# Kernel tuning notes

Measured on AMD Instinct MI355X. Metric: run time of the kernel, lower is better.

Reference implementation:

```python
import jax, jax.numpy as jnp
import numpy as np
import math

B, Q, CQ = 2, 2048, 512
H, D = 8, 64  # no_heads, c_hidden

def setup_inputs() -> dict:
    key = jax.random.key(0)
    ks = jax.random.split(key, 8)
    s = 0.02
    return {
        "q_x": jax.random.normal(ks[0], (B, Q, CQ), jnp.float32),
        "kv_x": jax.random.normal(ks[1], (B, Q, CQ), jnp.float32),
        "bias": jax.random.normal(ks[2], (B, 1, Q, Q), jnp.float32),
        "w_qkv": jax.random.normal(ks[3], (3 * H * D, CQ), jnp.float32) * s,
        "w_o": jax.random.normal(ks[4], (CQ, H * D), jnp.float32) * s,
        "b_o": jnp.zeros((CQ,), jnp.float32),
        "w_g": jax.random.normal(ks[5], (H * D, CQ), jnp.float32) * s,
        "b_g": jnp.zeros((H * D,), jnp.float32),
    }

def reference(q_x, kv_x, bias, w_qkv, w_o, b_o, w_g, b_g):
    # Fused QKV projection from q_x (kv_x is unused by the original module's _prep_qkv)
    qkv = jnp.einsum('bqc,ec->bqe', q_x, w_qkv)  # [B,Q,3*H*D]
    q, k, v = jnp.split(qkv, 3, axis=-1)
    q = q.reshape(B, Q, H, D) / math.sqrt(D)
    k = k.reshape(B, Q, H, D)
    v = v.reshape(B, Q, H, D)
    # scores + additive pairwise bias, softmax over keys
    scores = jnp.einsum('bqhd,bkhd->bhqk', q, k) + bias  # [B,H,Q,K]
    attn = jax.nn.softmax(scores, axis=-1)
    o = jnp.einsum('bhqk,bkhd->bqhd', attn, v)  # [B,Q,H,D]
    # sigmoid gating
    g = jax.nn.sigmoid(jnp.einsum('bqc,ec->bqe', q_x, w_g) + b_g).reshape(B, Q, H, D)
    o = o * g
    # output projection
    o = o.reshape(B, Q, H * D)
    return jnp.einsum('bqe,ce->bqc', o, w_o) + b_o
```

## Files before the change

### kernel.cpp

```cpp
#include <hip/hip_runtime.h>
#include <math.h>

#define B_  2
#define Q_  2048
#define CQ_ 512
#define H_  8
#define D_  64
#define M_  (B_*Q_)
#define L2E 1.44269504088896f

typedef __bf16 bf16;
typedef __bf16 bf16x4 __attribute__((ext_vector_type(4)));
typedef __bf16 bf16x8 __attribute__((ext_vector_type(8)));
typedef float  f32x4  __attribute__((ext_vector_type(4)));
typedef float  f32x16 __attribute__((ext_vector_type(16)));
typedef unsigned int u32x2 __attribute__((ext_vector_type(2)));

__device__ __forceinline__ void gl_lds16(const bf16* g, bf16* l) {
    __builtin_amdgcn_global_load_lds(
        (const __attribute__((address_space(1))) unsigned int*)g,
        (__attribute__((address_space(3))) unsigned int*)l, 16, 0, 0);
}

__device__ __forceinline__ unsigned int cvtpk_bf16(float lo, float hi) {
    unsigned int r;
    asm("v_cvt_pk_bf16_f32 %0, %1, %2" : "=v"(r) : "v"(lo), "v"(hi));
    return r;
}

#define S0 (4096*512)
#define S1 (1536*512)
#define S2 (512*512)
#define S3 (512*512)
__global__ __launch_bounds__(256)
void convert_kernel(const float* __restrict__ qx, const float* __restrict__ wqkv,
                    const float* __restrict__ wg, const float* __restrict__ wo,
                    bf16* __restrict__ qxb, bf16* __restrict__ wcat, bf16* __restrict__ wob)
{
    const long long t = (long long)blockIdx.x * 256 + threadIdx.x;
    const long long e = t * 8;
    const float* src; bf16* dst;
    if (e < S0)                { src = qx + e;                  dst = qxb + e; }
    else if (e < S0 + S1)      { src = wqkv + (e - S0);         dst = wcat + (e - S0); }
    else if (e < S0 + S1 + S2) { src = wg + (e - S0 - S1);      dst = wcat + S1 + (e - S0 - S1); }
    else                       { src = wo + (e - S0 - S1 - S2); dst = wob + (e - S0 - S1 - S2); }
    const float4 a = *(const float4*)(src);
    const float4 b = *(const float4*)(src + 4);
    bf16x8 v;
    v[0] = (bf16)a.x; v[1] = (bf16)a.y; v[2] = (bf16)a.z; v[3] = (bf16)a.w;
    v[4] = (bf16)b.x; v[5] = (bf16)b.y; v[6] = (bf16)b.z; v[7] = (bf16)b.w;
    *(bf16x8*)dst = v;
}

template<int BM, int BN, int EPI>
__global__ __launch_bounds__(256)
void gemm_bf16(const bf16* __restrict__ A, const bf16* __restrict__ W,
               const float* __restrict__ bvec, float* __restrict__ fout,
               bf16* __restrict__ qb, bf16* __restrict__ kb, bf16* __restrict__ vb,
               bf16* __restrict__ gb)
{
    constexpr int MI = BM / 32, NJ = BN / 32;
    __shared__ __align__(16) bf16 As[BM * 32];
    __shared__ __align__(16) bf16 Bs[BN * 32];

    const int t = threadIdx.x;
    const int w = t >> 6, lane = t & 63;
    const int l15 = lane & 15, quad = lane >> 4;
    const int wm = w & 1, wn = w >> 1;
    const int bm = blockIdx.x * BM;
    const int bn = blockIdx.y * BN;
    const bool swapped = (EPI == 1) || ((bn >> 9) != 2);

    f32x4 acc[MI][NJ] = {};

    const int rr = t >> 2;
    const int cc = (t & 3) * 8;

    for (int k0 = 0; k0 < 512; k0 += 32) {
        #pragma unroll
        for (int i = 0; i < BM / 64; ++i)
            gl_lds16(A + (size_t)(bm + i * 64 + rr) * 512 + k0 + cc,
                     As + (i * 64 + w * 16) * 32);
        #pragma unroll
        for (int i = 0; i < BN / 64; ++i)
            gl_lds16(W + (size_t)(bn + i * 64 + rr) * 512 + k0 + cc,
                     Bs + (i * 64 + w * 16) * 32);
        __asm__ volatile("s_waitcnt vmcnt(0)" ::: "memory");
        __syncthreads();

        bf16x8 af[MI], bfr[NJ];
        #pragma unroll
        for (int i = 0; i < MI; ++i)
            af[i] = *(const bf16x8*)(As + (wm * (BM / 2) + i * 16 + l15) * 32 + quad * 8);
        #pragma unroll
        for (int j = 0; j < NJ; ++j)
            bfr[j] = *(const bf16x8*)(Bs + (wn * (BN / 2) + j * 16 + l15) * 32 + quad * 8);
        if (swapped) {
            #pragma unroll
            for (int i = 0; i < MI; ++i)
                #pragma unroll
                for (int j = 0; j < NJ; ++j)
                    acc[i][j] = __builtin_amdgcn_mfma_f32_16x16x32_bf16(bfr[j], af[i], acc[i][j], 0, 0, 0);
        } else {
            #pragma unroll
            for (int i = 0; i < MI; ++i)
                #pragma unroll
                for (int j = 0; j < NJ; ++j)
                    acc[i][j] = __builtin_amdgcn_mfma_f32_16x16x32_bf16(af[i], bfr[j], acc[i][j], 0, 0, 0);
        }
        __syncthreads();
    }

    if (swapped) {
        #pragma unroll
        for (int i = 0; i < MI; ++i) {
            const int m = bm + wm * (BM / 2) + i * 16 + l15;
            const int b = m >> 11, qq = m & 2047;
            #pragma unroll
            for (int j = 0; j < NJ; ++j) {
                const int n0 = bn + wn * (BN / 2) + j * 16 + quad * 4;
                const f32x4 cv = acc[i][j];
                if constexpr (EPI == 1) {
                    float4 st;
                    st.x = cv[0] + bvec[n0 + 0];
                    st.y = cv[1] + bvec[n0 + 1];
                    st.z = cv[2] + bvec[n0 + 2];
                    st.w = cv[3] + bvec[n0 + 3];
                    *(float4*)(fout + (size_t)m * 512 + n0) = st;
                } else {
                    const int part = n0 >> 9;
                    if (part == 0) {
                        const int h = (n0 >> 6) & 7, d0 = n0 & 63;
                        bf16x4 q4;
                        #pragma unroll
                        for (int r = 0; r < 4; ++r) q4[r] = (bf16)(cv[r] * (0.125f * L2E));
                        *(bf16x4*)(qb + (size_t)(b * H_ + h) * (Q_ * D_) + (size_t)qq * 64 + d0) = q4;
                    } else if (part == 1) {
                        const int h = (n0 >> 6) & 7, d0 = n0 & 63;
                        const size_t off = (size_t)(b * H_ + h) * (Q_ * D_)
                            + (qq >> 6) * 4096 + ((qq >> 5) & 1) * 2048
                            + (d0 >> 4) * 512 + ((d0 >> 3) & 1) * 256
                            + (qq & 31) * 8 + (d0 & 7);
                        bf16x4 k4;
                        #pragma unroll
                        for (int r = 0; r < 4; ++r) k4[r] = (bf16)cv[r];
                        *(bf16x4*)(kb + off) = k4;
                    } else {
                        const int gcol = n0 & 511;
                        const float4 bv4 = *(const float4*)(bvec + gcol);
                        bf16x4 g4;
                        g4[0] = (bf16)(1.f / (1.f + __expf(-(cv[0] + bv4.x))));
                        g4[1] = (bf16)(1.f / (1.f + __expf(-(cv[1] + bv4.y))));
                        g4[2] = (bf16)(1.f / (1.f + __expf(-(cv[2] + bv4.z))));
                        g4[3] = (bf16)(1.f / (1.f + __expf(-(cv[3] + bv4.w))));
                        *(bf16x4*)(gb + (size_t)m * 512 + gcol) = g4;
                    }
                }
            }
        }
    } else {
        #pragma unroll
        for (int i = 0; i < MI; ++i) {
            const int m0 = bm + wm * (BM / 2) + i * 16 + quad * 4;
            const int b = m0 >> 11, qq0 = m0 & 2047;
            #pragma unroll
            for (int j = 0; j < NJ; ++j) {
                const int n = bn + wn * (BN / 2) + j * 16 + l15;
                const int h = (n >> 6) & 7, d = n & 63;
                const size_t off = (size_t)(b * H_ + h) * (Q_ * D_)
                    + (qq0 >> 6) * 4096 + (d >> 5) * 2048
                    + ((qq0 & 63) >> 4) * 512 + ((qq0 >> 3) & 1) * 256
                    + (d & 31) * 8 + (qq0 & 7);
                bf16x4 v4;
                #pragma unroll
                for (int r = 0; r < 4; ++r) v4[r] = (bf16)acc[i][j][r];
                *(bf16x4*)(vb + off) = v4;
            }
        }
    }
}

__global__ __launch_bounds__(256, 3)
void attn_part(const bf16* __restrict__ qb, const bf16* __restrict__ kf,
               const bf16* __restrict__ vf, const float* __restrict__ bias,
               bf16* __restrict__ po, float2* __restrict__ ml)
{
    __shared__ __align__(16) bf16 Ks[2][4096];
    __shared__ __align__(16) bf16 Vs[2][4096];

    const int tid  = threadIdx.x;
    const int wv   = tid >> 6, lane = tid & 63;
    const int l31  = lane & 31, b5 = lane >> 5;
    const int x    = blockIdx.x;
    const int bh   = ((x & 7) << 1) | (x >> 3);
    const int b    = bh >> 3;
    const int qg   = blockIdx.y * 128 + wv * 32 + l31;
    const int ks   = blockIdx.z;
    const int t0   = ks * 11;
    const int nt   = (ks < 2) ? 11 : 10;

    const bf16* qp = qb + ((size_t)bh * Q_ + qg) * D_;
    bf16x8 bq[4];
    #pragma unroll
    for (int c = 0; c < 4; ++c)
        bq[c] = *(const bf16x8*)(qp + c * 16 + b5 * 8);

    f32x16 acc[2] = {};
    float m_run = -INFINITY, l_run = 0.f;

    const bf16*  kfb  = kf + (size_t)bh * (Q_ * D_) + (size_t)t0 * 4096;
    const bf16*  vfb  = vf + (size_t)bh * (Q_ * D_) + (size_t)t0 * 4096;
    const float* brow = bias + ((size_t)b * Q_ + qg) * Q_ + t0 * 64;

    f32x4 nb[8];

    #pragma unroll
    for (int p = 0; p < 2; ++p) {
        gl_lds16(kfb + (wv * 2 + p) * 512 + lane * 8, Ks[0] + (wv * 2 + p) * 512);
        gl_lds16(vfb + (wv * 2 + p) * 512 + lane * 8, Vs[0] + (wv * 2 + p) * 512);
    }
    #pragma unroll
    for (int i = 0; i < 8; ++i)
        nb[i] = *(const f32x4*)(brow + (i >> 2) * 32 + (i & 3) * 8 + b5 * 4);
    __asm__ volatile("s_waitcnt vmcnt(0)" ::: "memory");
    __syncthreads();

    int cur = 0;
    #pragma unroll 1
    for (int t = 0; t < nt; ++t) {
        if (t < nt - 1) {
            const size_t off = (size_t)(t + 1) * 4096;
            #pragma unroll
            for (int p = 0; p < 2; ++p) {
                gl_lds16(kfb + off + (wv * 2 + p) * 512 + lane * 8,
                         Ks[cur ^ 1] + (wv * 2 + p) * 512);
                gl_lds16(vfb + off + (wv * 2 + p) * 512 + lane * 8,
                         Vs[cur ^ 1] + (wv * 2 + p) * 512);
            }
        }
        __asm__ volatile("" ::: "memory");

        f32x16 sv[2];
        #pragma unroll
        for (int kg = 0; kg < 2; ++kg)
            #pragma unroll
            for (int r = 0; r < 16; ++r)
                sv[kg][r] = nb[kg * 4 + (r >> 2)][r & 3] * L2E;

        if (t < nt - 1) {
            const int k0n = (t + 1) * 64;
            #pragma unroll
            for (int i = 0; i < 8; ++i)
                nb[i] = *(const f32x4*)(brow + k0n + (i >> 2) * 32 + (i & 3) * 8 + b5 * 4);
        }
        __asm__ volatile("" ::: "memory");

        const bf16* Kc = Ks[cur];
        __builtin_amdgcn_s_setprio(1);
        #pragma unroll
        for (int kg = 0; kg < 2; ++kg)
            #pragma unroll
            for (int c = 0; c < 4; ++c) {
                const bf16x8 ak = *(const bf16x8*)(Kc + kg * 2048 + c * 512 + lane * 8);
                sv[kg] = __builtin_amdgcn_mfma_f32_32x32x16_bf16(ak, bq[c], sv[kg], 0, 0, 0);
            }
        __builtin_amdgcn_s_setprio(0);

        float mx[16];
        #pragma unroll
        for (int r = 0; r < 16; ++r) mx[r] = fmaxf(sv[0][r], sv[1][r]);
        #pragma unroll
        for (int r = 0; r < 8; ++r) mx[r] = fmaxf(mx[r], mx[r + 8]);
        #pragma unroll
        for (int r = 0; r < 4; ++r) mx[r] = fmaxf(mx[r], mx[r + 4]);
        float tmax = fmaxf(fmaxf(mx[0], mx[1]), fmaxf(mx[2], mx[3]));
        tmax = fmaxf(tmax, __shfl_xor(tmax, 32, 64));

        const float mn = fmaxf(m_run, tmax);
        const float alpha = __builtin_amdgcn_exp2f(m_run - mn);
        m_run = mn;

        #pragma unroll
        for (int kg = 0; kg < 2; ++kg)
            #pragma unroll
            for (int r = 0; r < 16; ++r)
                sv[kg][r] = __builtin_amdgcn_exp2f(sv[kg][r] - mn);

        float sm[16];
        #pragma unroll
        for (int r = 0; r < 16; ++r) sm[r] = sv[0][r] + sv[1][r];
        #pragma unroll
        for (int r = 0; r < 8; ++r) sm[r] += sm[r + 8];
        #pragma unroll
        for (int r = 0; r < 4; ++r) sm[r] += sm[r + 4];
        float rsum = (sm[0] + sm[1]) + (sm[2] + sm[3]);
        rsum += __shfl_xor(rsum, 32, 64);
        l_run = l_run * alpha + rsum;
        acc[0] *= alpha;
        acc[1] *= alpha;

        bf16x8 bp[4];
        #pragma unroll
        for (int kg = 0; kg < 2; ++kg)
            #pragma unroll
            for (int h = 0; h < 2; ++h) {
                const unsigned int u  = cvtpk_bf16(sv[kg][8 * h + 0], sv[kg][8 * h + 1]);
                const unsigned int u2 = cvtpk_bf16(sv[kg][8 * h + 2], sv[kg][8 * h + 3]);
                const unsigned int vv = cvtpk_bf16(sv[kg][8 * h + 4], sv[kg][8 * h + 5]);
                const unsigned int v2 = cvtpk_bf16(sv[kg][8 * h + 6], sv[kg][8 * h + 7]);
                const u32x2 s1 = __builtin_amdgcn_permlane32_swap(u,  vv, false, false);
                const u32x2 s2 = __builtin_amdgcn_permlane32_swap(u2, v2, false, false);
                union { unsigned int w[4]; bf16x8 v8; } pkw;
                pkw.w[0] = s1[0]; pkw.w[1] = s2[0]; pkw.w[2] = s1[1]; pkw.w[3] = s2[1];
                bp[kg * 2 + h] = pkw.v8;
            }

        const bf16* Vc = Vs[cur];
        __builtin_amdgcn_s_setprio(1);
        #pragma unroll
        for (int c4 = 0; c4 < 4; ++c4) {
            #pragma unroll
            for (int dg = 0; dg < 2; ++dg) {
                const bf16x8 av = *(const bf16x8*)(Vc + dg * 2048 + c4 * 512 + lane * 8);
                acc[dg] = __builtin_amdgcn_mfma_f32_32x32x16_bf16(av, bp[c4], acc[dg], 0, 0, 0);
            }
        }
        __builtin_amdgcn_s_setprio(0);

        __asm__ volatile("s_waitcnt vmcnt(8)" ::: "memory");
        __syncthreads();
        cur ^= 1;
    }

    const float inv = 1.f / l_run;
    const size_t pbase = ((size_t)(ks * 16 + bh) * Q_ + qg) * 64;
    #pragma unroll
    for (int dg = 0; dg < 2; ++dg)
        #pragma unroll
        for (int gi = 0; gi < 4; ++gi) {
            const int d0 = dg * 32 + gi * 8 + b5 * 4;
            bf16x4 ov;
            #pragma unroll
            for (int r = 0; r < 4; ++r)
                ov[r] = (bf16)(acc[dg][gi * 4 + r] * inv);
            *(bf16x4*)(po + pbase + d0) = ov;
        }
    if (b5 == 0)
        ml[(size_t)(ks * 16 + bh) * Q_ + qg] = make_float2(m_run, l_run);
}

__global__ __launch_bounds__(256)
void merge_kernel(const bf16* __restrict__ po, const float2* __restrict__ ml,
                  const bf16* __restrict__ g, bf16* __restrict__ og)
{
    const int gid = blockIdx.x * 256 + threadIdx.x;
    const int row = gid >> 3;
    const int d8  = (gid & 7) * 8;
    const int bh  = row >> 11, qg = row & 2047;
    const int b   = bh >> 3, h = bh & 7;

    float2 m4[3];
    #pragma unroll
    for (int s = 0; s < 3; ++s) m4[s] = ml[(size_t)s * (16 * Q_) + row];
    const float M = fmaxf(fmaxf(m4[0].x, m4[1].x), m4[2].x);
    float w[3], tot = 0.f;
    #pragma unroll
    for (int s = 0; s < 3; ++s) {
        w[s] = m4[s].y * __builtin_amdgcn_exp2f(m4[s].x - M);
        tot += w[s];
    }
    const float inv = 1.f / tot;
    #pragma unroll
    for (int s = 0; s < 3; ++s) w[s] *= inv;

    bf16x8 o[3];
    #pragma unroll
    for (int s = 0; s < 3; ++s)
        o[s] = *(const bf16x8*)(po + (size_t)s * (16 * Q_ * 64) + (size_t)row * 64 + d8);

    const size_t obase = ((size_t)(b * Q_ + qg)) * 512 + h * 64 + d8;
    const bf16x8 gv = *(const bf16x8*)(g + obase);
    bf16x8 ov;
    #pragma unroll
    for (int r = 0; r < 8; ++r) {
        float acc = 0.f;
        #pragma unroll
        for (int s = 0; s < 3; ++s) acc += (float)o[s][r] * w[s];
        ov[r] = (bf16)(acc * (float)gv[r]);
    }
    *(bf16x8*)(og + obase) = ov;
}

extern "C" void kernel_launch(void* const* d_in, const int* in_sizes, int n_in,
                              void* d_out, int out_size, void* d_ws, size_t ws_size,
                              hipStream_t stream)
{
    const float* q_x   = (const float*)d_in[0];
    const float* bias  = (const float*)d_in[2];
    const float* w_qkv = (const float*)d_in[3];
    const float* w_o   = (const float*)d_in[4];
    const float* b_o   = (const float*)d_in[5];
    const float* w_g   = (const float*)d_in[6];
    const float* b_g   = (const float*)d_in[7];
    float* out = (float*)d_out;

    char* ws = (char*)d_ws;
    bf16*   qxb  = (bf16*)(ws);
    bf16*   wcat = (bf16*)(ws + (4u  << 20));
    bf16*   po   = (bf16*)(ws);
    bf16*   qb   = (bf16*)(ws + (16u << 20));
    bf16*   kb   = (bf16*)(ws + (20u << 20));
    bf16*   vb   = (bf16*)(ws + (24u << 20));
    bf16*   gb   = (bf16*)(ws + (28u << 20));
    bf16*   ogb  = (bf16*)(ws + (32u << 20));
    bf16*   wob  = (bf16*)(ws + (36u << 20));
    float2* ml   = (float2*)(ws + (36u << 20) + (1u << 19));

    convert_kernel<<<(S0 + S1 + S2 + S3) / (256 * 8), 256, 0, stream>>>(
        q_x, w_qkv, w_g, w_o, qxb, wcat, wob);
    gemm_bf16<128, 128, 0><<<dim3(32, 16), 256, 0, stream>>>(
        qxb, wcat, b_g, nullptr, qb, kb, vb, gb);
    attn_part<<<dim3(B_ * H_, Q_ / 128, 3), 256, 0, stream>>>(qb, kb, vb, bias, po, ml);
    merge_kernel<<<(16 * Q_ * 8) / 256, 256, 0, stream>>>(po, ml, gb, ogb);
    gemm_bf16<64, 128, 1><<<dim3(64, 4), 256, 0, stream>>>(
        ogb, wob, b_o, out, nullptr, nullptr, nullptr, nullptr);
}
```

Baseline: 178.3 us.

## Pre-rearrange bias into MFMA fragment order for coalesced attention loads

Adds a kernel that copies the fp32 bias into a tiled layout matching the MFMA accumulator fragment order, so each wave in the attention kernel reads each bias tile with contiguous per-lane float4 loads. Previously each lane read strided rows of the bias matrix, which gave poorly coalesced global loads repeated across all 8 heads. The cost is an extra 32 MB read and 32 MB write pass over the bias each call, plus another kernel launch.

```diff
diff --git a/kernel.cpp b/kernel.cpp
--- a/kernel.cpp
+++ b/kernel.cpp
@@ -50,6 +50,32 @@
     v[0] = (bf16)a.x; v[1] = (bf16)a.y; v[2] = (bf16)a.z; v[3] = (bf16)a.w;
     v[4] = (bf16)b.x; v[5] = (bf16)b.y; v[6] = (bf16)b.z; v[7] = (bf16)b.w;
     *(bf16x8*)dst = v;
+}
+
+__global__ __launch_bounds__(256)
+void bias_rearrange(const float* __restrict__ bias, float* __restrict__ bT)
+{
+    __shared__ float lds[2048];
+    const int x = blockIdx.x;
+    const int b = x >> 11, q32 = (x >> 5) & 63, kt = x & 31;
+    const int t = threadIdx.x;
+    const int qo = t >> 3, kc = (t & 7) * 8;
+    const float* src = bias + ((size_t)b * Q_ + q32 * 32 + qo) * Q_ + kt * 64 + kc;
+    const float4 a = *(const float4*)src;
+    const float4 c = *(const float4*)(src + 4);
+    const float v[8] = {a.x, a.y, a.z, a.w, c.x, c.y, c.z, c.w};
+    #pragma unroll
+    for (int j2 = 0; j2 < 8; ++j2) {
+        const int ko = kc + j2;
+        const int i  = (ko >> 5) * 4 + ((ko >> 3) & 3);
+        const int b5 = (ko >> 2) & 1;
+        const int j  = ko & 3;
+        lds[i * 256 + b5 * 128 + qo * 4 + j] = v[j2];
+    }
+    __syncthreads();
+    float* outp = bT + ((size_t)(b * 64 + q32) * 32 + kt) * 2048 + t * 8;
+    *(float4*)(outp)     = *(const float4*)(lds + t * 8);
+    *(float4*)(outp + 4) = *(const float4*)(lds + t * 8 + 4);
 }
 
 template<int BM, int BN, int EPI>
@@ -182,7 +208,7 @@
 
 __global__ __launch_bounds__(256, 3)
 void attn_part(const bf16* __restrict__ qb, const bf16* __restrict__ kf,
-               const bf16* __restrict__ vf, const float* __restrict__ bias,
+               const bf16* __restrict__ vf, const float* __restrict__ bT,
                bf16* __restrict__ po, float2* __restrict__ ml)
 {
     __shared__ __align__(16) bf16 Ks[2][4096];
@@ -210,7 +236,8 @@
 
     const bf16*  kfb  = kf + (size_t)bh * (Q_ * D_) + (size_t)t0 * 4096;
     const bf16*  vfb  = vf + (size_t)bh * (Q_ * D_) + (size_t)t0 * 4096;
-    const float* brow = bias + ((size_t)b * Q_ + qg) * Q_ + t0 * 64;
+    const int q32 = blockIdx.y * 4 + wv;
+    const float* brow = bT + (((size_t)b * 64 + q32) * 32 + t0) * 2048;
 
     f32x4 nb[8];
 
@@ -221,7 +248,7 @@
     }
     #pragma unroll
     for (int i = 0; i < 8; ++i)
-        nb[i] = *(const f32x4*)(brow + (i >> 2) * 32 + (i & 3) * 8 + b5 * 4);
+        nb[i] = *(const f32x4*)(brow + i * 256 + lane * 4);
     __asm__ volatile("s_waitcnt vmcnt(0)" ::: "memory");
     __syncthreads();
 
@@ -248,10 +275,10 @@
                 sv[kg][r] = nb[kg * 4 + (r >> 2)][r & 3] * L2E;
 
         if (t < nt - 1) {
-            const int k0n = (t + 1) * 64;
+            const float* bnx = brow + (size_t)(t + 1) * 2048;
             #pragma unroll
             for (int i = 0; i < 8; ++i)
-                nb[i] = *(const f32x4*)(brow + k0n + (i >> 2) * 32 + (i & 3) * 8 + b5 * 4);
+                nb[i] = *(const f32x4*)(bnx + i * 256 + lane * 4);
         }
         __asm__ volatile("" ::: "memory");
 
@@ -415,12 +442,14 @@
     bf16*   ogb  = (bf16*)(ws + (32u << 20));
     bf16*   wob  = (bf16*)(ws + (36u << 20));
     float2* ml   = (float2*)(ws + (36u << 20) + (1u << 19));
+    float*  bT   = (float*)(ws + (38u << 20));
 
     convert_kernel<<<(S0 + S1 + S2 + S3) / (256 * 8), 256, 0, stream>>>(
         q_x, w_qkv, w_g, w_o, qxb, wcat, wob);
+    bias_rearrange<<<B_ * 64 * 32, 256, 0, stream>>>(bias, bT);
     gemm_bf16<128, 128, 0><<<dim3(32, 16), 256, 0, stream>>>(
         qxb, wcat, b_g, nullptr, qb, kb, vb, gb);
-    attn_part<<<dim3(B_ * H_, Q_ / 128, 3), 256, 0, stream>>>(qb, kb, vb, bias, po, ml);
+    attn_part<<<dim3(B_ * H_, Q_ / 128, 3), 256, 0, stream>>>(qb, kb, vb, bT, po, ml);
     merge_kernel<<<(16 * Q_ * 8) / 256, 256, 0, stream>>>(po, ml, gb, ogb);
     gemm_bf16<64, 128, 1><<<dim3(64, 4), 256, 0, stream>>>(
         ogb, wob, b_o, out, nullptr, nullptr, nullptr, nullptr);
```

New measurement: 178.8 us. Within noise of the previous version (+0.3%).
